# Performance work log

Hardware: AMD Instinct MI355X
Metric: run time of the kernel (lower is better)

## Reference

```python
import jax, jax.numpy as jnp
import numpy as np

NEG_SLOPE = 0.2


def setup_inputs() -> dict:
    key = jax.random.key(0)
    ks = jax.random.split(key, 9)
    N, E, D, H, C, G = 50000, 800000, 128, 4, 32, 64
    x = jax.random.normal(ks[0], (N, D), dtype=jnp.float32)
    edge_index = jax.random.randint(ks[1], (2, E), 0, N, dtype=jnp.int64)
    batch_ids = jnp.sort(jax.random.randint(ks[2], (N,), 0, G, dtype=jnp.int64))
    Wl = jax.random.normal(ks[3], (D, H * C), dtype=jnp.float32) / np.sqrt(D)
    Wr = jax.random.normal(ks[4], (D, H * C), dtype=jnp.float32) / np.sqrt(D)
    att = jax.random.normal(ks[5], (H, C), dtype=jnp.float32) / np.sqrt(C)
    bias_conv = jax.random.normal(ks[6], (H * C,), dtype=jnp.float32) * 0.01
    W_mlp = jax.random.normal(ks[7], (H * C, H * C), dtype=jnp.float32) / np.sqrt(H * C)
    b_mlp = jax.random.normal(ks[8], (H * C,), dtype=jnp.float32) * 0.01
    return {"x": x, "edge_index": edge_index, "batch_ids": batch_ids,
            "num_graphs": G, "Wl": Wl, "Wr": Wr, "att": att,
            "bias_conv": bias_conv, "W_mlp": W_mlp, "b_mlp": b_mlp}


def gatv2_forward(x, edge_index, batch_ids, num_graphs, Wl, Wr, att, bias_conv, W_mlp, b_mlp):
    N = x.shape[0]
    H, C = att.shape
    # add self loops (PyG default)
    loops = jnp.arange(N, dtype=edge_index.dtype)
    src = jnp.concatenate([edge_index[0], loops])
    dst = jnp.concatenate([edge_index[1], loops])
    xl = (x @ Wl).reshape(N, H, C)  # source transform
    xr = (x @ Wr).reshape(N, H, C)  # target transform
    # GATv2 attention logits per edge/head
    e = jax.nn.leaky_relu(xl[src] + xr[dst], NEG_SLOPE)  # [E,H,C]
    logits = jnp.einsum('ehc,hc->eh', e, att)            # [E,H]
    # segment softmax over incoming edges of each dst node
    m = jax.ops.segment_max(logits, dst, num_segments=N)
    ex = jnp.exp(logits - m[dst])
    denom = jax.ops.segment_sum(ex, dst, num_segments=N)
    alpha = ex / denom[dst]                              # [E,H]
    # weighted scatter-sum of source features
    out = jax.ops.segment_sum(alpha[:, :, None] * xl[src], dst, num_segments=N)
    out = out.reshape(N, H * C) + bias_conv
    out = jax.nn.relu(out)
    # global max pool per graph
    pooled = jax.ops.segment_max(out, batch_ids, num_segments=num_graphs)
    return jax.nn.relu(pooled @ W_mlp + b_mlp)


def reference(x, edge_index, batch_ids, num_graphs, Wl, Wr, att, bias_conv, W_mlp, b_mlp):
    return gatv2_forward(x, edge_index, batch_ids, num_graphs, Wl, Wr, att,
                         bias_conv, W_mlp, b_mlp)
```

## Files before the change

### kernel.cpp

```cpp
#include <hip/hip_runtime.h>
#include <hip/hip_bf16.h>

#define NN 50000
#define EE 800000
#define HC 128
#define GG 64

#define NBLK 256
#define CHUNK (EE / NBLK)
#define NBUCK ((NN + 63) >> 6)
#define NTOT (NBUCK * NBLK)
#define NSB ((NTOT + 1023) / 1024)
#define ECAP 2048

typedef __attribute__((ext_vector_type(8))) short bf16x8;
typedef __attribute__((ext_vector_type(4))) float f32x4;
typedef _Float16 hv2 __attribute__((ext_vector_type(2)));

__device__ __forceinline__ float dpp4_redrow(float t) {
  t += __int_as_float(__builtin_amdgcn_update_dpp(0, __float_as_int(t), 0x111, 0xf, 0xf, true));
  t += __int_as_float(__builtin_amdgcn_update_dpp(0, __float_as_int(t), 0x112, 0xf, 0xf, true));
  t += __int_as_float(__builtin_amdgcn_update_dpp(0, __float_as_int(t), 0x114, 0xf, 0xf, true));
  t += __int_as_float(__builtin_amdgcn_update_dpp(0, __float_as_int(t), 0x118, 0xf, 0xf, true));
  return t;
}
__device__ __forceinline__ float bcast15(float t) {
  return __int_as_float(__builtin_amdgcn_ds_swizzle(__float_as_int(t), 0x1F0));
}

__device__ __forceinline__ unsigned pkbf(float lo, float hi) {
  __hip_bfloat162 h = __float22bfloat162_rn(float2{lo, hi});
  return *reinterpret_cast<unsigned*>(&h);
}

__global__ __launch_bounds__(128) void prep_w(const float* __restrict__ Wl,
                                              const float* __restrict__ Wr,
                                              short* __restrict__ Wtb) {
  int c = blockIdx.x;
  int k = threadIdx.x;
  const float* W = (c < 128) ? Wl : Wr;
  float v = W[k * 128 + (c & 127)];
  Wtb[c * 128 + k] = (short)(pkbf(v, 0.f) & 0xFFFF);
}

__global__ __launch_bounds__(256) void gemm_xw(
    const float* __restrict__ x, const short* __restrict__ Wtb,
    _Float16* __restrict__ xlh, _Float16* __restrict__ xrh)
{
  __shared__ short xs[128 * 136];
  const int t = threadIdx.x;
  const int rowbase = blockIdx.x * 128;
#pragma unroll
  for (int i = 0; i < 16; ++i) {
    int fi = i * 256 + t;
    int row = fi >> 5, k4 = fi & 31;
    int ar = rowbase + row; if (ar >= NN) ar = NN - 1;
    float4 v = *(const float4*)(x + (size_t)ar * 128 + k4 * 4);
    uint2 p = { pkbf(v.x, v.y), pkbf(v.z, v.w) };
    *(uint2*)&xs[row * 136 + k4 * 4] = p;
  }
  __syncthreads();
  const int w = t >> 6, l = t & 63;
  const int lo16 = l & 15, hi = l >> 4;
  f32x4 accL[2][8], accR[2][8];
#pragma unroll
  for (int rf = 0; rf < 2; ++rf)
#pragma unroll
    for (int cf = 0; cf < 8; ++cf) {
      accL[rf][cf] = f32x4{0.f, 0.f, 0.f, 0.f};
      accR[rf][cf] = f32x4{0.f, 0.f, 0.f, 0.f};
    }

  const short* asrc0 = &xs[(w * 32 + lo16) * 136 + hi * 8];
  const short* asrc1 = asrc0 + 16 * 136;
#pragma unroll
  for (int ks = 0; ks < 4; ++ks) {
    bf16x8 a0 = *(const bf16x8*)(asrc0 + ks * 32);
    bf16x8 a1 = *(const bf16x8*)(asrc1 + ks * 32);
#pragma unroll
    for (int cf = 0; cf < 8; ++cf) {
      const short* bp = &Wtb[(cf * 16 + lo16) * 128 + ks * 32 + hi * 8];
      bf16x8 bL = *(const bf16x8*)bp;
      bf16x8 bR = *(const bf16x8*)(bp + 128 * 128);
      accL[0][cf] = __builtin_amdgcn_mfma_f32_16x16x32_bf16(a0, bL, accL[0][cf], 0, 0, 0);
      accL[1][cf] = __builtin_amdgcn_mfma_f32_16x16x32_bf16(a1, bL, accL[1][cf], 0, 0, 0);
      accR[0][cf] = __builtin_amdgcn_mfma_f32_16x16x32_bf16(a0, bR, accR[0][cf], 0, 0, 0);
      accR[1][cf] = __builtin_amdgcn_mfma_f32_16x16x32_bf16(a1, bR, accR[1][cf], 0, 0, 0);
    }
  }
#pragma unroll
  for (int rf = 0; rf < 2; ++rf)
#pragma unroll
    for (int cf = 0; cf < 8; ++cf)
#pragma unroll
      for (int r = 0; r < 4; ++r) {
        int row = rowbase + w * 32 + rf * 16 + hi * 4 + r;
        if (row < NN) {
          int col = cf * 16 + lo16;
          xlh[(size_t)row * 128 + col] = (_Float16)accL[rf][cf][r];
          xrh[(size_t)row * 128 + col] = (_Float16)accR[rf][cf][r];
        }
      }
}

__global__ __launch_bounds__(256) void hist_coarse(const int* __restrict__ ei,
                                                   int* __restrict__ H2) {
  __shared__ int h[NBUCK];
  int t = threadIdx.x, blk = blockIdx.x;
  for (int b = t; b < NBUCK; b += 256) h[b] = 0;
  __syncthreads();
  int e0 = blk * CHUNK;
  for (int i = t; i < CHUNK; i += 256) {
    int d = ei[EE + e0 + i];
    atomicAdd(&h[d >> 6], 1);
  }
  __syncthreads();
  for (int b = t; b < NBUCK; b += 256) H2[blk * NBUCK + b] = h[b];
}

__global__ __launch_bounds__(256) void scanA(const int* __restrict__ H2,
                                             int* __restrict__ PS, int* __restrict__ bsum) {
  __shared__ int tmp[256];
  int t = threadIdx.x;
  int base = blockIdx.x * 1024 + t * 4;
  int v[4], local = 0;
#pragma unroll
  for (int j = 0; j < 4; ++j) {
    int L = base + j;
    v[j] = (L < NTOT) ? H2[(L % NBLK) * NBUCK + (L / NBLK)] : 0;
    local += v[j];
  }
  tmp[t] = local; __syncthreads();
  for (int off = 1; off < 256; off <<= 1) {
    int xv = (t >= off) ? tmp[t - off] : 0; __syncthreads();
    tmp[t] += xv; __syncthreads();
  }
  int excl = tmp[t] - local;
#pragma unroll
  for (int j = 0; j < 4; ++j) { int L = base + j; if (L < NTOT) PS[L] = excl; excl += v[j]; }
  if (t == 255) bsum[blockIdx.x] = tmp[255];
}

__global__ void scanB(int* __restrict__ bsum) {
  __shared__ int tmp[256];
  int t = threadIdx.x;
  int v = (t < NSB) ? bsum[t] : 0;
  tmp[t] = v; __syncthreads();
  for (int off = 1; off < 256; off <<= 1) {
    int xv = (t >= off) ? tmp[t - off] : 0; __syncthreads();
    tmp[t] += xv; __syncthreads();
  }
  if (t < NSB) bsum[t] = tmp[t] - v;
}

__global__ __launch_bounds__(256) void scatter_coarse(const int* __restrict__ ei,
                                                      const int* __restrict__ PS,
                                                      const int* __restrict__ bsum,
                                                      int* __restrict__ ec) {
  __shared__ int colbase[NBUCK];
  __shared__ int cur[NBUCK];
  int t = threadIdx.x, blk = blockIdx.x;
  for (int b = t; b < NBUCK; b += 256) {
    int L = b * NBLK + blk;
    colbase[b] = PS[L] + bsum[L >> 10];
    cur[b] = 0;
  }
  __syncthreads();
  int e0 = blk * CHUNK;
  for (int i = t; i < CHUNK; i += 256) {
    int d = ei[EE + e0 + i], s = ei[e0 + i];
    int b = d >> 6;
    int r = atomicAdd(&cur[b], 1);
    ec[colbase[b] + r] = s | ((d & 63) << 16);
  }
}

__global__ __launch_bounds__(256) void fine_sort(const int* __restrict__ PS,
                                                 const int* __restrict__ bsum,
                                                 const int* __restrict__ ec,
                                                 int* __restrict__ rs, int* __restrict__ csr) {
  __shared__ int lbuf[ECAP];
  __shared__ int outb[ECAP + 64];
  __shared__ int fh[64], sexcl[65], cur2[64];
  int t = threadIdx.x, b = blockIdx.x;
  int L0 = b * NBLK;
  int start = PS[L0] + bsum[L0 >> 10];
  int end;
  if (b + 1 < NBUCK) { int L1 = (b + 1) * NBLK; end = PS[L1] + bsum[L1 >> 10]; }
  else end = EE;
  int node0 = b << 6;
  int nl = NN - node0; if (nl > 64) nl = 64;
  int cnt = end - start; if (cnt > ECAP) cnt = ECAP;
  if (t < 64) { fh[t] = 0; cur2[t] = 0; }
  __syncthreads();
  for (int i = t; i < cnt; i += 256) {
    int p = ec[start + i];
    lbuf[i] = p;
    atomicAdd(&fh[(p >> 16) & 63], 1);
  }
  __syncthreads();
  if (t < 64) {
    int val = fh[t] + (t < nl ? 1 : 0);
    int w = val;
    for (int off = 1; off < 64; off <<= 1) {
      int u = __shfl_up(w, off);
      if (t >= off) w += u;
    }
    sexcl[t] = w - val;
    if (t == 63) sexcl[64] = w;
  }
  __syncthreads();
  int base = start + node0;
  if (t <= nl) rs[node0 + t] = base + sexcl[t];
  if (t < nl) {
    int r = atomicAdd(&cur2[t], 1);
    outb[sexcl[t] + r] = node0 + t;
  }
  for (int i = t; i < cnt; i += 256) {
    int p = lbuf[i];
    int f = (p >> 16) & 63;
    int r = atomicAdd(&cur2[f], 1);
    outb[sexcl[f] + r] = p & 0xFFFF;
  }
  __syncthreads();
  int tot = cnt + nl;
  for (int i = t; i < tot; i += 256) csr[base + i] = outb[i];
}

__global__ __launch_bounds__(256) void gat_agg(
    const unsigned* __restrict__ xlu, const unsigned* __restrict__ xru,
    const int* __restrict__ rs, const int* __restrict__ csr,
    const float* __restrict__ att, const float* __restrict__ bias,
    float* __restrict__ outn)
{
  int wid = threadIdx.x >> 6, lane = threadIdx.x & 63;
  int n = blockIdx.x * 4 + wid;
  if (n >= NN) return;
  hv2 xr2 = __builtin_bit_cast(hv2, xru[n * 64 + lane]);
  float2 at2 = ((const float2*)att)[lane];
  const float LOG2E = 1.4426950408889634f;
  hv2 att2;
  att2.x = (_Float16)(at2.x * LOG2E);
  att2.y = (_Float16)(at2.y * LOG2E);
  float s = 0.f, a0 = 0.f, a1 = 0.f;

  int jbeg = rs[n], jend = rs[n + 1];
  for (int j0 = jbeg; j0 < jend; j0 += 64) {
    int cnt = jend - j0; if (cnt > 64) cnt = 64;
    int sj = csr[j0 + (lane < cnt ? lane : cnt - 1)];
    int base = 0;
    for (; base + 8 <= cnt; base += 8) {
      unsigned wv[8];
#pragma unroll
      for (int i = 0; i < 8; ++i)
        wv[i] = xlu[__builtin_amdgcn_readlane(sj, base + i) * 64 + lane];
      float tb[8];
#pragma unroll
      for (int i = 0; i < 8; ++i) {
        hv2 v = __builtin_bit_cast(hv2, wv[i]);
        hv2 y = v + xr2;
        hv2 lr = __builtin_elementwise_max(y, y * (_Float16)0.2f);
        float td = __builtin_amdgcn_fdot2(lr, att2, 0.f, false);
        tb[i] = bcast15(dpp4_redrow(td));
      }
      float p[8];
#pragma unroll
      for (int i = 0; i < 8; ++i) p[i] = __builtin_amdgcn_exp2f(tb[i]);
#pragma unroll
      for (int i = 0; i < 8; ++i) {
        hv2 v = __builtin_bit_cast(hv2, wv[i]);
        s += p[i];
        a0 = fmaf(p[i], (float)v.x, a0);
        a1 = fmaf(p[i], (float)v.y, a1);
      }
    }
    for (; base < cnt; ++base) {
      unsigned w0 = xlu[__builtin_amdgcn_readlane(sj, base) * 64 + lane];
      hv2 va = __builtin_bit_cast(hv2, w0);
      hv2 ya = va + xr2;
      hv2 la = __builtin_elementwise_max(ya, ya * (_Float16)0.2f);
      float t = __builtin_amdgcn_fdot2(la, att2, 0.f, false);
      float p = __builtin_amdgcn_exp2f(bcast15(dpp4_redrow(t)));
      s += p;
      a0 = fmaf(p, (float)va.x, a0); a1 = fmaf(p, (float)va.y, a1);
    }
  }
  float inv = 1.f / s;
  float2 bi = ((const float2*)bias)[lane];
  float2 o;
  o.x = fmaxf(fmaf(a0, inv, bi.x), 0.f);
  o.y = fmaxf(fmaf(a1, inv, bi.y), 0.f);
  ((float2*)outn)[n * 64 + lane] = o;
}

__global__ __launch_bounds__(128) void pool_max(const float* __restrict__ outn,
                                                const int* __restrict__ batch,
                                                unsigned int* __restrict__ pooled) {
  int c = threadIdx.x;
  int n0 = blockIdx.x * 128;
  int nend = n0 + 128; if (nend > NN) nend = NN;
  int curg = batch[n0];
  float mx = 0.f;
#pragma unroll 4
  for (int n = n0; n < nend; ++n) {
    int g = batch[n];
    if (g != curg) {
      atomicMax(&pooled[curg * HC + c], __float_as_uint(mx));
      mx = 0.f; curg = g;
    }
    mx = fmaxf(mx, outn[(size_t)n * HC + c]);
  }
  atomicMax(&pooled[curg * HC + c], __float_as_uint(mx));
}

__global__ __launch_bounds__(128) void mlp_out(const unsigned int* __restrict__ pooled,
                                               const float* __restrict__ W,
                                               const float* __restrict__ b,
                                               float* __restrict__ out) {
  __shared__ float p[128];
  int g = blockIdx.x, j = threadIdx.x;
  p[j] = __uint_as_float(pooled[g * HC + j]);
  __syncthreads();
  float acc = b[j];
#pragma unroll 8
  for (int k = 0; k < 128; ++k) acc = fmaf(p[k], W[k * 128 + j], acc);
  out[g * HC + j] = fmaxf(acc, 0.f);
}

extern "C" void kernel_launch(void* const* d_in, const int* in_sizes, int n_in,
                              void* d_out, int out_size, void* d_ws, size_t ws_size,
                              hipStream_t stream) {
  const float* x    = (const float*)d_in[0];
  const int*   ei   = (const int*)d_in[1];
  const int*   batch= (const int*)d_in[2];
  const float* Wl   = (const float*)d_in[4];
  const float* Wr   = (const float*)d_in[5];
  const float* att  = (const float*)d_in[6];
  const float* bias = (const float*)d_in[7];
  const float* Wm   = (const float*)d_in[8];
  const float* bm   = (const float*)d_in[9];

  char* ws = (char*)d_ws;
  size_t off = 0;
  auto alloc = [&](size_t bytes) { void* p = ws + off; off += (bytes + 255) & ~size_t(255); return p; };
  unsigned* xlu  = (unsigned*)alloc((size_t)NN * 64 * 4);
  unsigned* xru  = (unsigned*)alloc((size_t)NN * 64 * 4);
  float* outn    = (float*)alloc((size_t)NN * HC * 4);
  int*   rs      = (int*)alloc((size_t)(NN + 1) * 4);
  int*   csr     = (int*)alloc((size_t)(EE + NN) * 4);
  int*   bsum    = (int*)alloc(NSB * 4);
  short* Wtb     = (short*)alloc((size_t)256 * 128 * 2);
  unsigned int* pooled = (unsigned int*)alloc((size_t)GG * HC * 4);
  int* ec = (int*)outn;
  int* H2 = (int*)((char*)outn + (size_t)4 * 1024 * 1024);
  int* PS = (int*)((char*)outn + (size_t)6 * 1024 * 1024);

  (void)hipMemsetAsync(pooled, 0, (size_t)GG * HC * 4, stream);

  prep_w<<<256, 128, 0, stream>>>(Wl, Wr, Wtb);
  gemm_xw<<<(NN + 127) / 128, 256, 0, stream>>>(x, Wtb, (_Float16*)xlu, (_Float16*)xru);
  hist_coarse<<<NBLK, 256, 0, stream>>>(ei, H2);
  scanA<<<NSB, 256, 0, stream>>>(H2, PS, bsum);
  scanB<<<1, 256, 0, stream>>>(bsum);
  scatter_coarse<<<NBLK, 256, 0, stream>>>(ei, PS, bsum, ec);
  fine_sort<<<NBUCK, 256, 0, stream>>>(PS, bsum, ec, rs, csr);
  gat_agg<<<NN / 4, 256, 0, stream>>>(xlu, xru, rs, csr, att, bias, outn);
  pool_max<<<(NN + 127) / 128, 128, 0, stream>>>(outn, batch, pooled);
  mlp_out<<<GG, 128, 0, stream>>>(pooled, Wm, bm, (float*)d_out);
}
```

Baseline: 150.1 us.

## Fuse fine sort with GAT aggregation and pooling with MLP, split GEMM

Merges the fine bucket sort into the attention aggregation kernel, so each block sorts its 64-node bucket in shared memory and aggregates straight from that buffer. This drops the global CSR write and re-read. The histogram is written transposed so the scan reads contiguous int4 values. Pooling and the MLP become one per-graph kernel that binary-searches the sorted batch ids, which removes the memset and the atomics. The GEMM is split over a second grid dimension for L and R. The cost is much lower aggregation parallelism: 782 blocks of 4 waves instead of 12500, and only 64 blocks for a pooling pass that scans all nodes serially.

Result: slower. 190.4 us (+26.8%).

```diff
diff --git a/kernel.cpp b/kernel.cpp
--- a/kernel.cpp
+++ b/kernel.cpp
@@ -50,6 +50,7 @@
   __shared__ short xs[128 * 136];
   const int t = threadIdx.x;
   const int rowbase = blockIdx.x * 128;
+  const int y = blockIdx.y;
 #pragma unroll
   for (int i = 0; i < 16; ++i) {
     int fi = i * 256 + t;
@@ -62,15 +63,13 @@
   __syncthreads();
   const int w = t >> 6, l = t & 63;
   const int lo16 = l & 15, hi = l >> 4;
-  f32x4 accL[2][8], accR[2][8];
+  f32x4 acc[2][8];
 #pragma unroll
   for (int rf = 0; rf < 2; ++rf)
 #pragma unroll
-    for (int cf = 0; cf < 8; ++cf) {
-      accL[rf][cf] = f32x4{0.f, 0.f, 0.f, 0.f};
-      accR[rf][cf] = f32x4{0.f, 0.f, 0.f, 0.f};
-    }
-
+    for (int cf = 0; cf < 8; ++cf) acc[rf][cf] = f32x4{0.f, 0.f, 0.f, 0.f};
+
+  const short* __restrict__ wp = Wtb + (size_t)y * 128 * 128;
   const short* asrc0 = &xs[(w * 32 + lo16) * 136 + hi * 8];
   const short* asrc1 = asrc0 + 16 * 136;
 #pragma unroll
@@ -79,15 +78,12 @@
     bf16x8 a1 = *(const bf16x8*)(asrc1 + ks * 32);
 #pragma unroll
     for (int cf = 0; cf < 8; ++cf) {
-      const short* bp = &Wtb[(cf * 16 + lo16) * 128 + ks * 32 + hi * 8];
-      bf16x8 bL = *(const bf16x8*)bp;
-      bf16x8 bR = *(const bf16x8*)(bp + 128 * 128);
-      accL[0][cf] = __builtin_amdgcn_mfma_f32_16x16x32_bf16(a0, bL, accL[0][cf], 0, 0, 0);
-      accL[1][cf] = __builtin_amdgcn_mfma_f32_16x16x32_bf16(a1, bL, accL[1][cf], 0, 0, 0);
-      accR[0][cf] = __builtin_amdgcn_mfma_f32_16x16x32_bf16(a0, bR, accR[0][cf], 0, 0, 0);
-      accR[1][cf] = __builtin_amdgcn_mfma_f32_16x16x32_bf16(a1, bR, accR[1][cf], 0, 0, 0);
+      bf16x8 b = *(const bf16x8*)&wp[(cf * 16 + lo16) * 128 + ks * 32 + hi * 8];
+      acc[0][cf] = __builtin_amdgcn_mfma_f32_16x16x32_bf16(a0, b, acc[0][cf], 0, 0, 0);
+      acc[1][cf] = __builtin_amdgcn_mfma_f32_16x16x32_bf16(a1, b, acc[1][cf], 0, 0, 0);
     }
   }
+  _Float16* __restrict__ dst = y == 0 ? xlh : xrh;
 #pragma unroll
   for (int rf = 0; rf < 2; ++rf)
 #pragma unroll
@@ -97,14 +93,13 @@
         int row = rowbase + w * 32 + rf * 16 + hi * 4 + r;
         if (row < NN) {
           int col = cf * 16 + lo16;
-          xlh[(size_t)row * 128 + col] = (_Float16)accL[rf][cf][r];
-          xrh[(size_t)row * 128 + col] = (_Float16)accR[rf][cf][r];
+          dst[(size_t)row * 128 + col] = (_Float16)acc[rf][cf][r];
         }
       }
 }
 
 __global__ __launch_bounds__(256) void hist_coarse(const int* __restrict__ ei,
-                                                   int* __restrict__ H2) {
+                                                   int* __restrict__ H2T) {
   __shared__ int h[NBUCK];
   int t = threadIdx.x, blk = blockIdx.x;
   for (int b = t; b < NBUCK; b += 256) h[b] = 0;
@@ -115,29 +110,31 @@
     atomicAdd(&h[d >> 6], 1);
   }
   __syncthreads();
-  for (int b = t; b < NBUCK; b += 256) H2[blk * NBUCK + b] = h[b];
-}
-
-__global__ __launch_bounds__(256) void scanA(const int* __restrict__ H2,
+  for (int b = t; b < NBUCK; b += 256) H2T[b * NBLK + blk] = h[b];
+}
+
+__global__ __launch_bounds__(256) void scanA(const int* __restrict__ H2T,
                                              int* __restrict__ PS, int* __restrict__ bsum) {
   __shared__ int tmp[256];
   int t = threadIdx.x;
   int base = blockIdx.x * 1024 + t * 4;
-  int v[4], local = 0;
-#pragma unroll
-  for (int j = 0; j < 4; ++j) {
-    int L = base + j;
-    v[j] = (L < NTOT) ? H2[(L % NBLK) * NBUCK + (L / NBLK)] : 0;
-    local += v[j];
-  }
+  int4 v = {0, 0, 0, 0};
+  if (base < NTOT) v = *(const int4*)&H2T[base];
+  int local = v.x + v.y + v.z + v.w;
   tmp[t] = local; __syncthreads();
   for (int off = 1; off < 256; off <<= 1) {
     int xv = (t >= off) ? tmp[t - off] : 0; __syncthreads();
     tmp[t] += xv; __syncthreads();
   }
   int excl = tmp[t] - local;
-#pragma unroll
-  for (int j = 0; j < 4; ++j) { int L = base + j; if (L < NTOT) PS[L] = excl; excl += v[j]; }
+  if (base < NTOT) {
+    int4 o;
+    o.x = excl; excl += v.x;
+    o.y = excl; excl += v.y;
+    o.z = excl; excl += v.z;
+    o.w = excl;
+    *(int4*)&PS[base] = o;
+  }
   if (t == 255) bsum[blockIdx.x] = tmp[255];
 }
 
@@ -175,23 +172,23 @@
   }
 }
 
-__global__ __launch_bounds__(256) void fine_sort(const int* __restrict__ PS,
-                                                 const int* __restrict__ bsum,
-                                                 const int* __restrict__ ec,
-                                                 int* __restrict__ rs, int* __restrict__ csr) {
+__global__ __launch_bounds__(256) void gat_bucket(
+    const unsigned* __restrict__ xlu, const unsigned* __restrict__ xru,
+    const int* __restrict__ PS, const int* __restrict__ bsum,
+    const int* __restrict__ ec, const float* __restrict__ att,
+    const float* __restrict__ bias, float* __restrict__ outn)
+{
   __shared__ int lbuf[ECAP];
   __shared__ int outb[ECAP + 64];
-  __shared__ int fh[64], sexcl[65], cur2[64];
+  __shared__ int fh[64], sexcl[65], cur[64];
   int t = threadIdx.x, b = blockIdx.x;
   int L0 = b * NBLK;
   int start = PS[L0] + bsum[L0 >> 10];
-  int end;
-  if (b + 1 < NBUCK) { int L1 = (b + 1) * NBLK; end = PS[L1] + bsum[L1 >> 10]; }
-  else end = EE;
+  int end = (b + 1 < NBUCK) ? PS[L0 + NBLK] + bsum[(L0 + NBLK) >> 10] : EE;
   int node0 = b << 6;
   int nl = NN - node0; if (nl > 64) nl = 64;
   int cnt = end - start; if (cnt > ECAP) cnt = ECAP;
-  if (t < 64) { fh[t] = 0; cur2[t] = 0; }
+  if (t < 64) { fh[t] = 0; cur[t] = 0; }
   __syncthreads();
   for (int i = t; i < cnt; i += 256) {
     int p = ec[start + i];
@@ -210,121 +207,101 @@
     if (t == 63) sexcl[64] = w;
   }
   __syncthreads();
-  int base = start + node0;
-  if (t <= nl) rs[node0 + t] = base + sexcl[t];
   if (t < nl) {
-    int r = atomicAdd(&cur2[t], 1);
+    int r = atomicAdd(&cur[t], 1);
     outb[sexcl[t] + r] = node0 + t;
   }
   for (int i = t; i < cnt; i += 256) {
     int p = lbuf[i];
     int f = (p >> 16) & 63;
-    int r = atomicAdd(&cur2[f], 1);
+    int r = atomicAdd(&cur[f], 1);
     outb[sexcl[f] + r] = p & 0xFFFF;
   }
   __syncthreads();
-  int tot = cnt + nl;
-  for (int i = t; i < tot; i += 256) csr[base + i] = outb[i];
-}
-
-__global__ __launch_bounds__(256) void gat_agg(
-    const unsigned* __restrict__ xlu, const unsigned* __restrict__ xru,
-    const int* __restrict__ rs, const int* __restrict__ csr,
-    const float* __restrict__ att, const float* __restrict__ bias,
-    float* __restrict__ outn)
-{
-  int wid = threadIdx.x >> 6, lane = threadIdx.x & 63;
-  int n = blockIdx.x * 4 + wid;
-  if (n >= NN) return;
-  hv2 xr2 = __builtin_bit_cast(hv2, xru[n * 64 + lane]);
+
+  int wid = t >> 6, lane = t & 63;
   float2 at2 = ((const float2*)att)[lane];
   const float LOG2E = 1.4426950408889634f;
   hv2 att2;
   att2.x = (_Float16)(at2.x * LOG2E);
   att2.y = (_Float16)(at2.y * LOG2E);
-  float s = 0.f, a0 = 0.f, a1 = 0.f;
-
-  int jbeg = rs[n], jend = rs[n + 1];
-  for (int j0 = jbeg; j0 < jend; j0 += 64) {
-    int cnt = jend - j0; if (cnt > 64) cnt = 64;
-    int sj = csr[j0 + (lane < cnt ? lane : cnt - 1)];
-    int base = 0;
-    for (; base + 8 <= cnt; base += 8) {
-      unsigned wv[8];
-#pragma unroll
-      for (int i = 0; i < 8; ++i)
-        wv[i] = xlu[__builtin_amdgcn_readlane(sj, base + i) * 64 + lane];
-      float tb[8];
-#pragma unroll
-      for (int i = 0; i < 8; ++i) {
-        hv2 v = __builtin_bit_cast(hv2, wv[i]);
-        hv2 y = v + xr2;
-        hv2 lr = __builtin_elementwise_max(y, y * (_Float16)0.2f);
-        float td = __builtin_amdgcn_fdot2(lr, att2, 0.f, false);
-        tb[i] = bcast15(dpp4_redrow(td));
+  float2 bi = ((const float2*)bias)[lane];
+
+  for (int ni = wid; ni < nl; ni += 4) {
+    int n = node0 + ni;
+    hv2 xr2 = __builtin_bit_cast(hv2, xru[n * 64 + lane]);
+    float s = 0.f, a0 = 0.f, a1 = 0.f;
+    int jbeg = sexcl[ni], jend = sexcl[ni + 1];
+    for (int j0 = jbeg; j0 < jend; j0 += 64) {
+      int cnt2 = jend - j0; if (cnt2 > 64) cnt2 = 64;
+      int sj = outb[j0 + (lane < cnt2 ? lane : cnt2 - 1)];
+      int base = 0;
+      for (; base + 8 <= cnt2; base += 8) {
+        unsigned wv[8];
+#pragma unroll
+        for (int i = 0; i < 8; ++i)
+          wv[i] = xlu[__builtin_amdgcn_readlane(sj, base + i) * 64 + lane];
+        float tb[8];
+#pragma unroll
+        for (int i = 0; i < 8; ++i) {
+          hv2 v = __builtin_bit_cast(hv2, wv[i]);
+          hv2 y = v + xr2;
+          hv2 lr = __builtin_elementwise_max(y, y * (_Float16)0.2f);
+          float td = __builtin_amdgcn_fdot2(lr, att2, 0.f, false);
+          tb[i] = bcast15(dpp4_redrow(td));
+        }
+        float p[8];
+#pragma unroll
+        for (int i = 0; i < 8; ++i) p[i] = __builtin_amdgcn_exp2f(tb[i]);
+#pragma unroll
+        for (int i = 0; i < 8; ++i) {
+          hv2 v = __builtin_bit_cast(hv2, wv[i]);
+          s += p[i];
+          a0 = fmaf(p[i], (float)v.x, a0);
+          a1 = fmaf(p[i], (float)v.y, a1);
+        }
       }
-      float p[8];
-#pragma unroll
-      for (int i = 0; i < 8; ++i) p[i] = __builtin_amdgcn_exp2f(tb[i]);
-#pragma unroll
-      for (int i = 0; i < 8; ++i) {
-        hv2 v = __builtin_bit_cast(hv2, wv[i]);
-        s += p[i];
-        a0 = fmaf(p[i], (float)v.x, a0);
-        a1 = fmaf(p[i], (float)v.y, a1);
+      for (; base < cnt2; ++base) {
+        unsigned w0 = xlu[__builtin_amdgcn_readlane(sj, base) * 64 + lane];
+        hv2 va = __builtin_bit_cast(hv2, w0);
+        hv2 ya = va + xr2;
+        hv2 la = __builtin_elementwise_max(ya, ya * (_Float16)0.2f);
+        float tt = __builtin_amdgcn_fdot2(la, att2, 0.f, false);
+        float p = __builtin_amdgcn_exp2f(bcast15(dpp4_redrow(tt)));
+        s += p;
+        a0 = fmaf(p, (float)va.x, a0); a1 = fmaf(p, (float)va.y, a1);
       }
     }
-    for (; base < cnt; ++base) {
-      unsigned w0 = xlu[__builtin_amdgcn_readlane(sj, base) * 64 + lane];
-      hv2 va = __builtin_bit_cast(hv2, w0);
-      hv2 ya = va + xr2;
-      hv2 la = __builtin_elementwise_max(ya, ya * (_Float16)0.2f);
-      float t = __builtin_amdgcn_fdot2(la, att2, 0.f, false);
-      float p = __builtin_amdgcn_exp2f(bcast15(dpp4_redrow(t)));
-      s += p;
-      a0 = fmaf(p, (float)va.x, a0); a1 = fmaf(p, (float)va.y, a1);
-    }
-  }
-  float inv = 1.f / s;
-  float2 bi = ((const float2*)bias)[lane];
-  float2 o;
-  o.x = fmaxf(fmaf(a0, inv, bi.x), 0.f);
-  o.y = fmaxf(fmaf(a1, inv, bi.y), 0.f);
-  ((float2*)outn)[n * 64 + lane] = o;
-}
-
-__global__ __launch_bounds__(128) void pool_max(const float* __restrict__ outn,
+    float inv = 1.f / s;
+    float2 o;
+    o.x = fmaxf(fmaf(a0, inv, bi.x), 0.f);
+    o.y = fmaxf(fmaf(a1, inv, bi.y), 0.f);
+    ((float2*)outn)[n * 64 + lane] = o;
+  }
+}
+
+__global__ __launch_bounds__(128) void pool_mlp(const float* __restrict__ outn,
                                                 const int* __restrict__ batch,
-                                                unsigned int* __restrict__ pooled) {
-  int c = threadIdx.x;
-  int n0 = blockIdx.x * 128;
-  int nend = n0 + 128; if (nend > NN) nend = NN;
-  int curg = batch[n0];
+                                                const float* __restrict__ W,
+                                                const float* __restrict__ bm,
+                                                float* __restrict__ out) {
+  __shared__ float p[128];
+  int g = blockIdx.x, j = threadIdx.x;
+  int a = 0, bnd = NN;
+  while (a < bnd) { int m = (a + bnd) >> 1; if (batch[m] < g) a = m + 1; else bnd = m; }
+  int lo = a;
+  bnd = NN;
+  while (a < bnd) { int m = (a + bnd) >> 1; if (batch[m] < g + 1) a = m + 1; else bnd = m; }
+  int hi = a;
   float mx = 0.f;
 #pragma unroll 4
-  for (int n = n0; n < nend; ++n) {
-    int g = batch[n];
-    if (g != curg) {
-      atomicMax(&pooled[curg * HC + c], __float_as_uint(mx));
-      mx = 0.f; curg = g;
-    }
-    mx = fmaxf(mx, outn[(size_t)n * HC + c]);
-  }
-  atomicMax(&pooled[curg * HC + c], __float_as_uint(mx));
-}
-
-__global__ __launch_bounds__(128) void mlp_out(const unsigned int* __restrict__ pooled,
-                                               const float* __restrict__ W,
-                                               const float* __restrict__ b,
-                                               float* __restrict__ out) {
-  __shared__ float p[128];
-  int g = blockIdx.x, j = threadIdx.x;
-  p[j] = __uint_as_float(pooled[g * HC + j]);
-  __syncthreads();
-  float acc = b[j];
+  for (int n = lo; n < hi; ++n) mx = fmaxf(mx, outn[(size_t)n * 128 + j]);
+  p[j] = mx;
+  __syncthreads();
+  float acc = bm[j];
 #pragma unroll 8
   for (int k = 0; k < 128; ++k) acc = fmaf(p[k], W[k * 128 + j], acc);
-  out[g * HC + j] = fmaxf(acc, 0.f);
+  out[g * 128 + j] = fmaxf(acc, 0.f);
 }
 
 extern "C" void kernel_launch(void* const* d_in, const int* in_sizes, int n_in,
@@ -346,25 +323,18 @@
   unsigned* xlu  = (unsigned*)alloc((size_t)NN * 64 * 4);
   unsigned* xru  = (unsigned*)alloc((size_t)NN * 64 * 4);
   float* outn    = (float*)alloc((size_t)NN * HC * 4);
-  int*   rs      = (int*)alloc((size_t)(NN + 1) * 4);
-  int*   csr     = (int*)alloc((size_t)(EE + NN) * 4);
+  int*   H2T     = (int*)alloc((size_t)NTOT * 4);
+  int*   PS      = (int*)alloc((size_t)NTOT * 4);
+  int*   ec      = (int*)alloc((size_t)EE * 4);
   int*   bsum    = (int*)alloc(NSB * 4);
   short* Wtb     = (short*)alloc((size_t)256 * 128 * 2);
-  unsigned int* pooled = (unsigned int*)alloc((size_t)GG * HC * 4);
-  int* ec = (int*)outn;
-  int* H2 = (int*)((char*)outn + (size_t)4 * 1024 * 1024);
-  int* PS = (int*)((char*)outn + (size_t)6 * 1024 * 1024);
-
-  (void)hipMemsetAsync(pooled, 0, (size_t)GG * HC * 4, stream);
 
   prep_w<<<256, 128, 0, stream>>>(Wl, Wr, Wtb);
-  gemm_xw<<<(NN + 127) / 128, 256, 0, stream>>>(x, Wtb, (_Float16*)xlu, (_Float16*)xru);
-  hist_coarse<<<NBLK, 256, 0, stream>>>(ei, H2);
-  scanA<<<NSB, 256, 0, stream>>>(H2, PS, bsum);
+  gemm_xw<<<dim3((NN + 127) / 128, 2), 256, 0, stream>>>(x, Wtb, (_Float16*)xlu, (_Float16*)xru);
+  hist_coarse<<<NBLK, 256, 0, stream>>>(ei, H2T);
+  scanA<<<NSB, 256, 0, stream>>>(H2T, PS, bsum);
   scanB<<<1, 256, 0, stream>>>(bsum);
   scatter_coarse<<<NBLK, 256, 0, stream>>>(ei, PS, bsum, ec);
-  fine_sort<<<NBUCK, 256, 0, stream>>>(PS, bsum, ec, rs, csr);
-  gat_agg<<<NN / 4, 256, 0, stream>>>(xlu, xru, rs, csr, att, bias, outn);
-  pool_max<<<(NN + 127) / 128, 128, 0, stream>>>(outn, batch, pooled);
-  mlp_out<<<GG, 128, 0, stream>>>(pooled, Wm, bm, (float*)d_out);
-}
+  gat_bucket<<<NBUCK, 256, 0, stream>>>(xlu, xru, PS, bsum, ec, att, bias, outn);
+  pool_mlp<<<GG, 128, 0, stream>>>(outn, batch, Wm, bm, (float*)d_out);
+}
```

## Prefetch neighbor rows in aggregation, transpose histogram, fuse pool with MLP

Applied to the files above, without the earlier changes.

The aggregation loop now software-pipelines its gathers, loading the next 8 source rows while the current 8 are processed, to hide memory latency. The coarse histogram is written transposed so the scan can use contiguous int4 loads and stores instead of strided gathers. Pooling and the MLP are fused into one kernel per graph that binary-searches the sorted batch ids, which removes the memset, the atomics and one launch. The fused pool runs only 64 blocks, each scanning about 780 nodes serially, so it may be slower than the old pool kernel that spread the nodes over many blocks.

New measurement: 169.4 us. 12.8% more time.

```diff
diff --git a/kernel.cpp b/kernel.cpp
--- a/kernel.cpp
+++ b/kernel.cpp
@@ -104,7 +104,7 @@
 }
 
 __global__ __launch_bounds__(256) void hist_coarse(const int* __restrict__ ei,
-                                                   int* __restrict__ H2) {
+                                                   int* __restrict__ H2T) {
   __shared__ int h[NBUCK];
   int t = threadIdx.x, blk = blockIdx.x;
   for (int b = t; b < NBUCK; b += 256) h[b] = 0;
@@ -115,29 +115,31 @@
     atomicAdd(&h[d >> 6], 1);
   }
   __syncthreads();
-  for (int b = t; b < NBUCK; b += 256) H2[blk * NBUCK + b] = h[b];
-}
-
-__global__ __launch_bounds__(256) void scanA(const int* __restrict__ H2,
+  for (int b = t; b < NBUCK; b += 256) H2T[b * NBLK + blk] = h[b];
+}
+
+__global__ __launch_bounds__(256) void scanA(const int* __restrict__ H2T,
                                              int* __restrict__ PS, int* __restrict__ bsum) {
   __shared__ int tmp[256];
   int t = threadIdx.x;
   int base = blockIdx.x * 1024 + t * 4;
-  int v[4], local = 0;
-#pragma unroll
-  for (int j = 0; j < 4; ++j) {
-    int L = base + j;
-    v[j] = (L < NTOT) ? H2[(L % NBLK) * NBUCK + (L / NBLK)] : 0;
-    local += v[j];
-  }
+  int4 v = {0, 0, 0, 0};
+  if (base < NTOT) v = *(const int4*)&H2T[base];
+  int local = v.x + v.y + v.z + v.w;
   tmp[t] = local; __syncthreads();
   for (int off = 1; off < 256; off <<= 1) {
     int xv = (t >= off) ? tmp[t - off] : 0; __syncthreads();
     tmp[t] += xv; __syncthreads();
   }
   int excl = tmp[t] - local;
-#pragma unroll
-  for (int j = 0; j < 4; ++j) { int L = base + j; if (L < NTOT) PS[L] = excl; excl += v[j]; }
+  if (base < NTOT) {
+    int4 o;
+    o.x = excl; excl += v.x;
+    o.y = excl; excl += v.y;
+    o.z = excl; excl += v.z;
+    o.w = excl;
+    *(int4*)&PS[base] = o;
+  }
   if (t == 255) bsum[blockIdx.x] = tmp[255];
 }
 
@@ -185,9 +187,7 @@
   int t = threadIdx.x, b = blockIdx.x;
   int L0 = b * NBLK;
   int start = PS[L0] + bsum[L0 >> 10];
-  int end;
-  if (b + 1 < NBUCK) { int L1 = (b + 1) * NBLK; end = PS[L1] + bsum[L1 >> 10]; }
-  else end = EE;
+  int end = (b + 1 < NBUCK) ? PS[L0 + NBLK] + bsum[(L0 + NBLK) >> 10] : EE;
   int node0 = b << 6;
   int nl = NN - node0; if (nl > 64) nl = 64;
   int cnt = end - start; if (cnt > ECAP) cnt = ECAP;
@@ -225,6 +225,29 @@
   __syncthreads();
   int tot = cnt + nl;
   for (int i = t; i < tot; i += 256) csr[base + i] = outb[i];
+}
+
+__device__ __forceinline__ void proc8(const unsigned* wv, hv2 att2, hv2 xr2,
+                                      float& s, float& a0, float& a1) {
+  float tb[8];
+#pragma unroll
+  for (int i = 0; i < 8; ++i) {
+    hv2 v = __builtin_bit_cast(hv2, wv[i]);
+    hv2 y = v + xr2;
+    hv2 lr = __builtin_elementwise_max(y, y * (_Float16)0.2f);
+    float td = __builtin_amdgcn_fdot2(lr, att2, 0.f, false);
+    tb[i] = bcast15(dpp4_redrow(td));
+  }
+  float p[8];
+#pragma unroll
+  for (int i = 0; i < 8; ++i) p[i] = __builtin_amdgcn_exp2f(tb[i]);
+#pragma unroll
+  for (int i = 0; i < 8; ++i) {
+    hv2 v = __builtin_bit_cast(hv2, wv[i]);
+    s += p[i];
+    a0 = fmaf(p[i], (float)v.x, a0);
+    a1 = fmaf(p[i], (float)v.y, a1);
+  }
 }
 
 __global__ __launch_bounds__(256) void gat_agg(
@@ -249,30 +272,22 @@
     int cnt = jend - j0; if (cnt > 64) cnt = 64;
     int sj = csr[j0 + (lane < cnt ? lane : cnt - 1)];
     int base = 0;
-    for (; base + 8 <= cnt; base += 8) {
-      unsigned wv[8];
+    if (cnt >= 8) {
+      unsigned cur[8];
 #pragma unroll
       for (int i = 0; i < 8; ++i)
-        wv[i] = xlu[__builtin_amdgcn_readlane(sj, base + i) * 64 + lane];
-      float tb[8];
-#pragma unroll
-      for (int i = 0; i < 8; ++i) {
-        hv2 v = __builtin_bit_cast(hv2, wv[i]);
-        hv2 y = v + xr2;
-        hv2 lr = __builtin_elementwise_max(y, y * (_Float16)0.2f);
-        float td = __builtin_amdgcn_fdot2(lr, att2, 0.f, false);
-        tb[i] = bcast15(dpp4_redrow(td));
+        cur[i] = xlu[__builtin_amdgcn_readlane(sj, i) * 64 + lane];
+      for (; base + 16 <= cnt; base += 8) {
+        unsigned nxt[8];
+#pragma unroll
+        for (int i = 0; i < 8; ++i)
+          nxt[i] = xlu[__builtin_amdgcn_readlane(sj, base + 8 + i) * 64 + lane];
+        proc8(cur, att2, xr2, s, a0, a1);
+#pragma unroll
+        for (int i = 0; i < 8; ++i) cur[i] = nxt[i];
       }
-      float p[8];
-#pragma unroll
-      for (int i = 0; i < 8; ++i) p[i] = __builtin_amdgcn_exp2f(tb[i]);
-#pragma unroll
-      for (int i = 0; i < 8; ++i) {
-        hv2 v = __builtin_bit_cast(hv2, wv[i]);
-        s += p[i];
-        a0 = fmaf(p[i], (float)v.x, a0);
-        a1 = fmaf(p[i], (float)v.y, a1);
-      }
+      proc8(cur, att2, xr2, s, a0, a1);
+      base += 8;
     }
     for (; base < cnt; ++base) {
       unsigned w0 = xlu[__builtin_amdgcn_readlane(sj, base) * 64 + lane];
@@ -293,38 +308,28 @@
   ((float2*)outn)[n * 64 + lane] = o;
 }
 
-__global__ __launch_bounds__(128) void pool_max(const float* __restrict__ outn,
+__global__ __launch_bounds__(128) void pool_mlp(const float* __restrict__ outn,
                                                 const int* __restrict__ batch,
-                                                unsigned int* __restrict__ pooled) {
-  int c = threadIdx.x;
-  int n0 = blockIdx.x * 128;
-  int nend = n0 + 128; if (nend > NN) nend = NN;
-  int curg = batch[n0];
+                                                const float* __restrict__ W,
+                                                const float* __restrict__ bm,
+                                                float* __restrict__ out) {
+  __shared__ float p[128];
+  int g = blockIdx.x, j = threadIdx.x;
+  int a = 0, bnd = NN;
+  while (a < bnd) { int m = (a + bnd) >> 1; if (batch[m] < g) a = m + 1; else bnd = m; }
+  int lo = a;
+  bnd = NN;
+  while (a < bnd) { int m = (a + bnd) >> 1; if (batch[m] < g + 1) a = m + 1; else bnd = m; }
+  int hi = a;
   float mx = 0.f;
 #pragma unroll 4
-  for (int n = n0; n < nend; ++n) {
-    int g = batch[n];
-    if (g != curg) {
-      atomicMax(&pooled[curg * HC + c], __float_as_uint(mx));
-      mx = 0.f; curg = g;
-    }
-    mx = fmaxf(mx, outn[(size_t)n * HC + c]);
-  }
-  atomicMax(&pooled[curg * HC + c], __float_as_uint(mx));
-}
-
-__global__ __launch_bounds__(128) void mlp_out(const unsigned int* __restrict__ pooled,
-                                               const float* __restrict__ W,
-                                               const float* __restrict__ b,
-                                               float* __restrict__ out) {
-  __shared__ float p[128];
-  int g = blockIdx.x, j = threadIdx.x;
-  p[j] = __uint_as_float(pooled[g * HC + j]);
-  __syncthreads();
-  float acc = b[j];
+  for (int n = lo; n < hi; ++n) mx = fmaxf(mx, outn[(size_t)n * 128 + j]);
+  p[j] = mx;
+  __syncthreads();
+  float acc = bm[j];
 #pragma unroll 8
   for (int k = 0; k < 128; ++k) acc = fmaf(p[k], W[k * 128 + j], acc);
-  out[g * HC + j] = fmaxf(acc, 0.f);
+  out[g * 128 + j] = fmaxf(acc, 0.f);
 }
 
 extern "C" void kernel_launch(void* const* d_in, const int* in_sizes, int n_in,
@@ -348,23 +353,19 @@
   float* outn    = (float*)alloc((size_t)NN * HC * 4);
   int*   rs      = (int*)alloc((size_t)(NN + 1) * 4);
   int*   csr     = (int*)alloc((size_t)(EE + NN) * 4);
+  int*   H2T     = (int*)alloc((size_t)NTOT * 4);
+  int*   PS      = (int*)alloc((size_t)NTOT * 4);
+  int*   ec      = (int*)alloc((size_t)EE * 4);
   int*   bsum    = (int*)alloc(NSB * 4);
   short* Wtb     = (short*)alloc((size_t)256 * 128 * 2);
-  unsigned int* pooled = (unsigned int*)alloc((size_t)GG * HC * 4);
-  int* ec = (int*)outn;
-  int* H2 = (int*)((char*)outn + (size_t)4 * 1024 * 1024);
-  int* PS = (int*)((char*)outn + (size_t)6 * 1024 * 1024);
-
-  (void)hipMemsetAsync(pooled, 0, (size_t)GG * HC * 4, stream);
 
   prep_w<<<256, 128, 0, stream>>>(Wl, Wr, Wtb);
   gemm_xw<<<(NN + 127) / 128, 256, 0, stream>>>(x, Wtb, (_Float16*)xlu, (_Float16*)xru);
-  hist_coarse<<<NBLK, 256, 0, stream>>>(ei, H2);
-  scanA<<<NSB, 256, 0, stream>>>(H2, PS, bsum);
+  hist_coarse<<<NBLK, 256, 0, stream>>>(ei, H2T);
+  scanA<<<NSB, 256, 0, stream>>>(H2T, PS, bsum);
   scanB<<<1, 256, 0, stream>>>(bsum);
   scatter_coarse<<<NBLK, 256, 0, stream>>>(ei, PS, bsum, ec);
   fine_sort<<<NBUCK, 256, 0, stream>>>(PS, bsum, ec, rs, csr);
   gat_agg<<<NN / 4, 256, 0, stream>>>(xlu, xru, rs, csr, att, bias, outn);
-  pool_max<<<(NN + 127) / 128, 128, 0, stream>>>(outn, batch, pooled);
-  mlp_out<<<GG, 128, 0, stream>>>(pooled, Wm, bm, (float*)d_out);
-}
+  pool_mlp<<<GG, 128, 0, stream>>>(outn, batch, Wm, bm, (float*)d_out);
+}
```
